# Performance work log

Measured on AMD Instinct MI355X. Metric: run time of the kernel, lower is better.

## Reference

```python
import math
import jax, jax.numpy as jnp
import numpy as np

N_HEAD = 16

def setup_inputs() -> dict:
    key = jax.random.key(0)
    k1, k2, k3 = jax.random.split(key, 3)
    B, T, C = 4, 2048, 1024
    x = jax.random.normal(k1, (B, T, C), dtype=jnp.float32)
    Wqkv = jax.random.normal(k2, (C, 3 * C), dtype=jnp.float32) * (1.0 / math.sqrt(C))
    bqkv = jnp.zeros((3 * C,), dtype=jnp.float32)
    Wproj = jax.random.normal(k3, (C, C), dtype=jnp.float32) * (1.0 / math.sqrt(C))
    bproj = jnp.zeros((C,), dtype=jnp.float32)
    return {"x": x, "Wqkv": Wqkv, "bqkv": bqkv, "Wproj": Wproj, "bproj": bproj}

def reference(x, Wqkv, bqkv, Wproj, bproj):
    B, T, C = x.shape
    H = N_HEAD
    D = C // H
    # fused QKV projection
    qkv = x @ Wqkv + bqkv                      # [B,T,3C]
    qkv = qkv.reshape(B, T, 3, H, D).transpose(0, 2, 3, 1, 4)  # [B,3,H,T,D]
    q, k, v = qkv[:, 0], qkv[:, 1], qkv[:, 2]  # each [B,H,T,D]
    scale = 1.0 / math.sqrt(D)
    att = jnp.einsum('bhtd,bhsd->bhts', q, k) * scale  # [B,H,T,T]
    # causal mask: disallow s > t
    mask = jnp.triu(jnp.ones((T, T), dtype=bool), k=1)
    att = jnp.where(mask, jnp.float32(-1e9), att)
    att = jax.nn.softmax(att, axis=-1)
    y = jnp.einsum('bhts,bhsd->bhtd', att, v)  # [B,H,T,D]
    y = y.transpose(0, 2, 1, 3).reshape(B, T, C)
    y = y @ Wproj + bproj
    return y
```

## Files before the change

kernel.cpp:

```cpp
#include <hip/hip_runtime.h>
#include <hip/hip_bf16.h>

#define B_ 4
#define T_ 2048
#define C_ 1024
#define H_ 16
#define D_ 64

typedef __attribute__((ext_vector_type(8))) short short8;
typedef __attribute__((ext_vector_type(4))) float f32x4;

#define QSCALE 0.18033688011112042f

static __device__ __forceinline__ unsigned short f2bf(float f) {
  unsigned u = __float_as_uint(f);
  u += 0x7fff + ((u >> 16) & 1);
  return (unsigned short)(u >> 16);
}

static __device__ __forceinline__ unsigned cvt_pk_bf16(float lo, float hi) {
  unsigned r;
  asm("v_cvt_pk_bf16_f32 %0, %1, %2" : "=v"(r) : "v"(lo), "v"(hi));
  return r;
}

static __device__ __forceinline__ float fast_exp2(float x) {
#if __has_builtin(__builtin_amdgcn_exp2f)
  return __builtin_amdgcn_exp2f(x);
#else
  return exp2f(x);
#endif
}

#define GL2LDS16(g, l)                                              \
  __builtin_amdgcn_global_load_lds(                                 \
      (const __attribute__((address_space(1))) void*)(g),           \
      (__attribute__((address_space(3))) void*)(l), 16, 0, 0)

__global__ __launch_bounds__(256) void prepass(
    const float* __restrict__ x, const float* __restrict__ Wq,
    const float* __restrict__ Wp, ushort* __restrict__ xb,
    ushort* __restrict__ Wqt, ushort* __restrict__ Wpt) {
  __shared__ ushort tile[32][33];
  const int bid = blockIdx.x;
  if (bid < 8192) {
    const size_t i = ((size_t)bid * 256 + threadIdx.x) * 4;
    float4 vv = *(const float4*)(x + i);
    ushort4 o = {f2bf(vv.x), f2bf(vv.y), f2bf(vv.z), f2bf(vv.w)};
    *(ushort4*)(xb + i) = o;
    return;
  }
  const float* in;
  ushort* out;
  int N, tix;
  if (bid < 8192 + 3072) {
    in = Wq; out = Wqt; N = 3 * C_; tix = bid - 8192;
  } else {
    in = Wp; out = Wpt; N = C_; tix = bid - 11264;
  }
  const int nT = N >> 5;
  const int k0 = (tix / nT) << 5, n0 = (tix % nT) << 5;
  const int r = threadIdx.x >> 3;
  const int c4 = (threadIdx.x & 7) << 2;
  float4 v = *(const float4*)(in + (size_t)(k0 + r) * N + n0 + c4);
  tile[c4 + 0][r] = f2bf(v.x);
  tile[c4 + 1][r] = f2bf(v.y);
  tile[c4 + 2][r] = f2bf(v.z);
  tile[c4 + 3][r] = f2bf(v.w);
  __syncthreads();
  ushort4 o = {tile[r][c4], tile[r][c4 + 1], tile[r][c4 + 2], tile[r][c4 + 3]};
  *(ushort4*)(out + (size_t)(n0 + r) * C_ + k0 + c4) = o;
}

static __device__ __forceinline__ void swz_src64(int wave, int lane, int p,
                                                 int& row, int& offU) {
  const int flat = p * 4096 + wave * 1024 + lane * 16;
  row = flat >> 7;
  const int pos = (flat & 127) >> 4;
  const int x = pos ^ (row & 7);
  offU = x * 8;
}
static __device__ __forceinline__ int swz_frag64(int r, int quad, int ko) {
  return r * 128 + (((quad | (ko << 2)) ^ (r & 7)) << 4);
}

__global__ __launch_bounds__(512, 2) void gemm_qkv_mfma(
    const ushort* __restrict__ A, const ushort* __restrict__ Bt,
    const float* __restrict__ bias, ushort* __restrict__ q,
    ushort* __restrict__ k, ushort* __restrict__ v) {
  __shared__ __align__(16) ushort KA[3][128 * 64];
  __shared__ __align__(16) ushort KB[3][256 * 64];
  const int wave = threadIdx.x >> 6, lane = threadIdx.x & 63;
  const int c = lane & 15, quad = lane >> 4;
  const int wm = wave >> 2, wn = wave & 3;
  const int bid0 = blockIdx.x;
  const int bid = (bid0 & 7) * 96 + (bid0 >> 3);
  const int m0 = (bid / 12) << 7;
  const int n0 = (bid % 12) << 8;

  int aRow[2], aX[2], bRow[4], bX[4];
#pragma unroll
  for (int p = 0; p < 2; ++p) {
    const int flat = p * 8192 + (int)threadIdx.x * 16;
    aRow[p] = flat >> 7;
    aX[p] = (((flat & 127) >> 4) ^ (aRow[p] & 7)) * 8;
  }
#pragma unroll
  for (int p = 0; p < 4; ++p) {
    const int flat = p * 8192 + (int)threadIdx.x * 16;
    bRow[p] = flat >> 7;
    bX[p] = (((flat & 127) >> 4) ^ (bRow[p] & 7)) * 8;
  }
  int fOffA[2][4], fOffB[2][4];
#pragma unroll
  for (int ko = 0; ko < 2; ++ko) {
#pragma unroll
    for (int i = 0; i < 4; ++i)
      fOffA[ko][i] = swz_frag64(wm * 64 + i * 16 + c, quad, ko);
#pragma unroll
    for (int j = 0; j < 4; ++j)
      fOffB[ko][j] = swz_frag64(wn * 64 + j * 16 + c, quad, ko);
  }

  f32x4 acc[4][4];
#pragma unroll
  for (int i = 0; i < 4; ++i)
#pragma unroll
    for (int j = 0; j < 4; ++j) acc[i][j] = (f32x4){0.f, 0.f, 0.f, 0.f};

#pragma unroll
  for (int p = 0; p < 4; ++p)
    GL2LDS16(Bt + (size_t)(n0 + bRow[p]) * C_ + bX[p],
             (char*)KB[0] + p * 8192 + wave * 1024);
#pragma unroll
  for (int p = 0; p < 2; ++p)
    GL2LDS16(A + (size_t)(m0 + aRow[p]) * C_ + aX[p],
             (char*)KA[0] + p * 8192 + wave * 1024);
#pragma unroll
  for (int p = 0; p < 4; ++p)
    GL2LDS16(Bt + (size_t)(n0 + bRow[p]) * C_ + 64 + bX[p],
             (char*)KB[1] + p * 8192 + wave * 1024);
#pragma unroll
  for (int p = 0; p < 2; ++p)
    GL2LDS16(A + (size_t)(m0 + aRow[p]) * C_ + 64 + aX[p],
             (char*)KA[1] + p * 8192 + wave * 1024);
  asm volatile("s_waitcnt vmcnt(6)" ::: "memory");
  __builtin_amdgcn_s_barrier();

  int cur = 0, s2 = 2;
  for (int kt = 0; kt < 16; ++kt) {
    const int kk2 = (kt + 2) << 6;
    const bool more = (kt + 2) < 16;
    const char* la = (const char*)KA[cur];
    const char* lb = (const char*)KB[cur];
    short8 af[4][2], bf0[2][2], bf1[2][2];

#pragma unroll
    for (int i = 0; i < 4; ++i)
#pragma unroll
      for (int ko = 0; ko < 2; ++ko) af[i][ko] = *(const short8*)(la + fOffA[ko][i]);
#pragma unroll
    for (int d = 0; d < 2; ++d)
#pragma unroll
      for (int ko = 0; ko < 2; ++ko) bf0[d][ko] = *(const short8*)(lb + fOffB[ko][d]);
    if (more) {
      GL2LDS16(Bt + (size_t)(n0 + bRow[0]) * C_ + kk2 + bX[0],
               (char*)KB[s2] + 0 * 8192 + wave * 1024);
      GL2LDS16(Bt + (size_t)(n0 + bRow[1]) * C_ + kk2 + bX[1],
               (char*)KB[s2] + 1 * 8192 + wave * 1024);
      GL2LDS16(A + (size_t)(m0 + aRow[0]) * C_ + kk2 + aX[0],
               (char*)KA[s2] + 0 * 8192 + wave * 1024);
    }
    __builtin_amdgcn_s_barrier();
    __builtin_amdgcn_s_setprio(1);
#pragma unroll
    for (int i = 0; i < 4; ++i)
#pragma unroll
      for (int dj = 0; dj < 2; ++dj)
#pragma unroll
        for (int ko = 0; ko < 2; ++ko)
          acc[i][dj] = __builtin_amdgcn_mfma_f32_16x16x32_bf16(
              af[i][ko], bf0[dj][ko], acc[i][dj], 0, 0, 0);
    __builtin_amdgcn_s_setprio(0);
    __builtin_amdgcn_s_barrier();

#pragma unroll
    for (int d = 0; d < 2; ++d)
#pragma unroll
      for (int ko = 0; ko < 2; ++ko)
        bf1[d][ko] = *(const short8*)(lb + fOffB[ko][2 + d]);
    if (more) {
      GL2LDS16(Bt + (size_t)(n0 + bRow[2]) * C_ + kk2 + bX[2],
               (char*)KB[s2] + 2 * 8192 + wave * 1024);
      GL2LDS16(Bt + (size_t)(n0 + bRow[3]) * C_ + kk2 + bX[3],
               (char*)KB[s2] + 3 * 8192 + wave * 1024);
      GL2LDS16(A + (size_t)(m0 + aRow[1]) * C_ + kk2 + aX[1],
               (char*)KA[s2] + 1 * 8192 + wave * 1024);
    }
    __builtin_amdgcn_s_barrier();
    __builtin_amdgcn_s_setprio(1);
#pragma unroll
    for (int i = 0; i < 4; ++i)
#pragma unroll
      for (int dj = 0; dj < 2; ++dj)
#pragma unroll
        for (int ko = 0; ko < 2; ++ko)
          acc[i][2 + dj] = __builtin_amdgcn_mfma_f32_16x16x32_bf16(
              af[i][ko], bf1[dj][ko], acc[i][2 + dj], 0, 0, 0);
    __builtin_amdgcn_s_setprio(0);
    __builtin_amdgcn_s_barrier();

    if (kt + 1 < 16) {
      if (more)
        asm volatile("s_waitcnt vmcnt(6)" ::: "memory");
      else
        asm volatile("s_waitcnt vmcnt(0)" ::: "memory");
      __builtin_amdgcn_s_barrier();
    }
    cur = (cur == 2) ? 0 : cur + 1;
    s2 = (s2 == 2) ? 0 : s2 + 1;
  }

  const int s = n0 >> 10;
  if (s == 2) {
#pragma unroll
    for (int j = 0; j < 4; ++j) {
      const int n = n0 + wn * 64 + j * 16 + c;
      const int h = (n >> 6) & 15, d = n & 63;
      const float bval = bias[n];
#pragma unroll
      for (int i = 0; i < 4; ++i) {
        const int m = m0 + wm * 64 + i * 16 + quad * 4;
        const int b = m >> 11, t = m & 2047;
        ushort4 pk = {f2bf(acc[i][j][0] + bval), f2bf(acc[i][j][1] + bval),
                      f2bf(acc[i][j][2] + bval), f2bf(acc[i][j][3] + bval)};
        *(ushort4*)(v + (((size_t)((b << 4) + h) << 6) + d) * T_ + t) = pk;
      }
    }
  } else {
    ushort* outp = (s == 0) ? q : k;
    const float sc = (s == 0) ? QSCALE : 1.0f;
#pragma unroll
    for (int j = 0; j < 4; ++j) {
      const int n = n0 + wn * 64 + j * 16 + c;
      const int h = (n >> 6) & 15, d = n & 63;
      const float bval = bias[n];
#pragma unroll
      for (int i = 0; i < 4; ++i) {
#pragma unroll
        for (int r = 0; r < 4; ++r) {
          const int m = m0 + wm * 64 + i * 16 + quad * 4 + r;
          const int b = m >> 11, t = m & 2047;
          outp[(((size_t)((b << 4) + h) << 11) + t) * 64 + d] =
              f2bf((acc[i][j][r] + bval) * sc);
        }
      }
    }
  }
}

__global__ __launch_bounds__(256) void gemm_proj_mfma(
    const ushort* __restrict__ A, const ushort* __restrict__ Bt,
    const float* __restrict__ bias, float* __restrict__ out) {
  __shared__ __align__(16) ushort As[128 * 64];
  __shared__ __align__(16) ushort Bs[128 * 64];
  const int tid = threadIdx.x;
  const int wave = tid >> 6, lane = tid & 63;
  const int c = lane & 15, quad = lane >> 4;
  const int wm = wave & 1, wn = wave >> 1;
  const int bid0 = blockIdx.y * 8 + blockIdx.x;
  const int bid = (bid0 & 7) * 64 + (bid0 >> 3);
  const int m0 = (bid >> 3) << 7;
  const int n0 = (bid & 7) << 7;

  int sRow[4], sOff[4];
#pragma unroll
  for (int p = 0; p < 4; ++p) swz_src64(wave, lane, p, sRow[p], sOff[p]);
  int fOffA[2][4], fOffB[2][4];
#pragma unroll
  for (int ko = 0; ko < 2; ++ko) {
#pragma unroll
    for (int i = 0; i < 4; ++i)
      fOffA[ko][i] = swz_frag64(wm * 64 + i * 16 + c, quad, ko);
#pragma unroll
    for (int j = 0; j < 4; ++j)
      fOffB[ko][j] = swz_frag64(wn * 64 + j * 16 + c, quad, ko);
  }

  f32x4 acc[4][4];
#pragma unroll
  for (int i = 0; i < 4; ++i)
#pragma unroll
    for (int j = 0; j < 4; ++j) acc[i][j] = (f32x4){0.f, 0.f, 0.f, 0.f};

  for (int k0 = 0; k0 < C_; k0 += 64) {
    __syncthreads();
#pragma unroll
    for (int p = 0; p < 4; ++p) {
      GL2LDS16(A + (size_t)(m0 + sRow[p]) * C_ + k0 + sOff[p],
               (char*)As + p * 4096 + wave * 1024);
      GL2LDS16(Bt + (size_t)(n0 + sRow[p]) * C_ + k0 + sOff[p],
               (char*)Bs + p * 4096 + wave * 1024);
    }
    __syncthreads();
#pragma unroll
    for (int ko = 0; ko < 2; ++ko) {
      short8 af[4], bf[4];
#pragma unroll
      for (int i = 0; i < 4; ++i)
        af[i] = *(const short8*)((const char*)As + fOffA[ko][i]);
#pragma unroll
      for (int j = 0; j < 4; ++j)
        bf[j] = *(const short8*)((const char*)Bs + fOffB[ko][j]);
#pragma unroll
      for (int i = 0; i < 4; ++i)
#pragma unroll
        for (int j = 0; j < 4; ++j)
          acc[i][j] = __builtin_amdgcn_mfma_f32_16x16x32_bf16(af[i], bf[j],
                                                              acc[i][j], 0, 0, 0);
    }
  }

#pragma unroll
  for (int j = 0; j < 4; ++j) {
    const int n = n0 + wn * 64 + j * 16 + c;
    const float bval = bias[n];
#pragma unroll
    for (int i = 0; i < 4; ++i) {
#pragma unroll
      for (int r = 0; r < 4; ++r) {
        const int m = m0 + wm * 64 + i * 16 + quad * 4 + r;
        out[(size_t)m * C_ + n] = acc[i][j][r] + bval;
      }
    }
  }
}

__global__ __launch_bounds__(256) void attn(const ushort* __restrict__ q,
                                            const ushort* __restrict__ k,
                                            const ushort* __restrict__ v,
                                            ushort* __restrict__ y2) {
  const int qt = 15 - (int)(blockIdx.x >> 6);
  const int bh = blockIdx.x & 63;
  const int t0 = qt << 7;
  const int w = threadIdx.x >> 6;
  const int lane = threadIdx.x & 63;
  const int c = lane & 15;
  const int quad = lane >> 4;

  const ushort* qp = q + (size_t)bh * T_ * D_;
  const ushort* kp = k + (size_t)bh * T_ * D_;
  const ushort* vp = v + (size_t)bh * D_ * T_;

  __shared__ __align__(16) ushort Ks[2][64 * 64];
  __shared__ __align__(16) ushort Vs[2][64 * 64];
  __shared__ __align__(16) ushort Ps[4][32][72];

  short8 qf[2][2];
#pragma unroll
  for (int g = 0; g < 2; ++g) {
    const ushort* qrow = qp + (size_t)(t0 + 32 * w + 16 * g + c) * D_;
    qf[g][0] = *(const short8*)(qrow + quad * 8);
    qf[g][1] = *(const short8*)(qrow + 32 + quad * 8);
  }

  int sRow[2], sX[2];
#pragma unroll
  for (int p = 0; p < 2; ++p) {
    const int flat = p * 4096 + (int)threadIdx.x * 16;
    sRow[p] = flat >> 7;
    sX[p] = (((flat & 127) >> 4) ^ (sRow[p] & 7)) * 8;
  }

#define STAGE(buf, s0s)                                                   \
  do {                                                                    \
    _Pragma("unroll") for (int p = 0; p < 2; ++p) {                       \
      GL2LDS16(kp + (size_t)((s0s) + sRow[p]) * D_ + sX[p],               \
               (char*)Ks[buf] + p * 4096 + w * 1024);                     \
      GL2LDS16(vp + (size_t)sRow[p] * T_ + (s0s) + sX[p],                 \
               (char*)Vs[buf] + p * 4096 + w * 1024);                     \
    }                                                                     \
  } while (0)

  f32x4 o[2][4];
  float l_i[2] = {0.f, 0.f};
#pragma unroll
  for (int g = 0; g < 2; ++g)
#pragma unroll
    for (int dt = 0; dt < 4; ++dt) o[g][dt] = (f32x4){0.f, 0.f, 0.f, 0.f};

  const int nb = 2 * qt + 2;
  STAGE(0, 0);
  int cur = 0;

  for (int ib = 0; ib < nb; ++ib) {
    const int s0 = ib << 6;
    __syncthreads();
    if (ib + 1 < nb) STAGE(cur ^ 1, s0 + 64);

    f32x4 st[2][4];
    __builtin_amdgcn_s_setprio(1);
#pragma unroll
    for (int kt = 0; kt < 4; ++kt) {
      const char* kb = (const char*)Ks[cur];
      short8 af0 = *(const short8*)(kb + swz_frag64(kt * 16 + c, quad, 0));
      short8 af1 = *(const short8*)(kb + swz_frag64(kt * 16 + c, quad, 1));
#pragma unroll
      for (int g = 0; g < 2; ++g) {
        f32x4 a = (f32x4){0.f, 0.f, 0.f, 0.f};
        a = __builtin_amdgcn_mfma_f32_16x16x32_bf16(af0, qf[g][0], a, 0, 0, 0);
        a = __builtin_amdgcn_mfma_f32_16x16x32_bf16(af1, qf[g][1], a, 0, 0, 0);
        st[g][kt] = a;
      }
    }
    __builtin_amdgcn_s_setprio(0);

#pragma unroll
    for (int g = 0; g < 2; ++g) {
      const int qbase = t0 + 32 * w + 16 * g;
      if (s0 + 63 > qbase) {
#pragma unroll
        for (int kt = 0; kt < 4; ++kt)
#pragma unroll
          for (int r = 0; r < 4; ++r)
            if (s0 + kt * 16 + 4 * quad + r > qbase + c) st[g][kt][r] = -1e30f;
      }
      float lacc = 0.f;
#pragma unroll
      for (int kt = 0; kt < 4; ++kt) {
        float p0 = fast_exp2(st[g][kt][0]);
        float p1 = fast_exp2(st[g][kt][1]);
        float p2 = fast_exp2(st[g][kt][2]);
        float p3 = fast_exp2(st[g][kt][3]);
        lacc += (p0 + p1) + (p2 + p3);
        uint2 pw = {cvt_pk_bf16(p0, p1), cvt_pk_bf16(p2, p3)};
        *(uint2*)(&Ps[w][g * 16 + c][kt * 16 + 4 * quad]) = pw;
      }
      l_i[g] += lacc;
    }

    short8 pf[2][2];
#pragma unroll
    for (int g = 0; g < 2; ++g) {
      pf[g][0] = *(const short8*)(&Ps[w][g * 16 + c][quad * 8]);
      pf[g][1] = *(const short8*)(&Ps[w][g * 16 + c][32 + quad * 8]);
    }
    __builtin_amdgcn_s_setprio(1);
#pragma unroll
    for (int dt = 0; dt < 4; ++dt) {
      const char* vb = (const char*)Vs[cur];
      short8 vf0 = *(const short8*)(vb + swz_frag64(dt * 16 + c, quad, 0));
      short8 vf1 = *(const short8*)(vb + swz_frag64(dt * 16 + c, quad, 1));
#pragma unroll
      for (int g = 0; g < 2; ++g) {
        o[g][dt] =
            __builtin_amdgcn_mfma_f32_16x16x32_bf16(vf0, pf[g][0], o[g][dt], 0, 0, 0);
        o[g][dt] =
            __builtin_amdgcn_mfma_f32_16x16x32_bf16(vf1, pf[g][1], o[g][dt], 0, 0, 0);
      }
    }
    __builtin_amdgcn_s_setprio(0);
    cur ^= 1;
  }
#undef STAGE

  float linv[2];
#pragma unroll
  for (int g = 0; g < 2; ++g) {
    float ls = l_i[g];
    ls += __shfl_xor(ls, 16);
    ls += __shfl_xor(ls, 32);
    linv[g] = 1.0f / ls;
  }

  const int b = bh >> 4, h = bh & 15;
#pragma unroll
  for (int g = 0; g < 2; ++g) {
    const int row = t0 + 32 * w + 16 * g + c;
    ushort* dst = y2 + (size_t)(b * T_ + row) * C_ + h * 64;
#pragma unroll
    for (int dt = 0; dt < 4; ++dt) {
      uint2 ov = {cvt_pk_bf16(o[g][dt][0] * linv[g], o[g][dt][1] * linv[g]),
                  cvt_pk_bf16(o[g][dt][2] * linv[g], o[g][dt][3] * linv[g])};
      *(uint2*)(dst + dt * 16 + 4 * quad) = ov;
    }
  }
}

extern "C" void kernel_launch(void* const* d_in, const int* in_sizes, int n_in,
                              void* d_out, int out_size, void* d_ws,
                              size_t ws_size, hipStream_t stream) {
  const float* x = (const float*)d_in[0];
  const float* Wqkv = (const float*)d_in[1];
  const float* bqkv = (const float*)d_in[2];
  const float* Wproj = (const float*)d_in[3];
  const float* bproj = (const float*)d_in[4];
  float* out = (float*)d_out;

  const size_t per = (size_t)B_ * H_ * T_ * D_;
  ushort* q = (ushort*)d_ws;
  ushort* k = q + per;
  ushort* v = k + per;
  ushort* y2 = v + per;
  ushort* xb = y2 + per;
  ushort* Wqkvt = xb + per;
  ushort* Wprojt = Wqkvt + 3 * C_ * C_;

  prepass<<<dim3(12288), 256, 0, stream>>>(x, Wqkv, Wproj, xb, Wqkvt, Wprojt);
  gemm_qkv_mfma<<<dim3(768), 512, 0, stream>>>(xb, Wqkvt, bqkv, q, k, v);
  attn<<<dim3(1024), 256, 0, stream>>>(q, k, v, y2);
  gemm_proj_mfma<<<dim3(8, 64), 256, 0, stream>>>(y2, Wprojt, bproj, out);
}
```

Measured before the change: 258.8 us.

## Double-buffer proj GEMM loads and shuffle P fragments instead of LDS roundtrip

The output-projection GEMM now double-buffers its A/B tiles in shared memory, so the next k-tile is prefetched while MFMAs run on the current one. It also raises wave priority around the MFMA block, and one barrier per iteration is removed. In the attention kernel, the softmax probability tile no longer goes through a per-wave LDS scratch buffer; the MFMA input fragments are rebuilt with cross-lane shuffles instead. The changes double the GEMM's LDS footprint, which may reduce occupancy, and add shuffle and select instructions in the attention inner loop.

```diff
diff --git a/kernel.cpp b/kernel.cpp
--- a/kernel.cpp
+++ b/kernel.cpp
@@ -262,8 +262,8 @@
 __global__ __launch_bounds__(256) void gemm_proj_mfma(
     const ushort* __restrict__ A, const ushort* __restrict__ Bt,
     const float* __restrict__ bias, float* __restrict__ out) {
-  __shared__ __align__(16) ushort As[128 * 64];
-  __shared__ __align__(16) ushort Bs[128 * 64];
+  __shared__ __align__(16) ushort As[2][128 * 64];
+  __shared__ __align__(16) ushort Bs[2][128 * 64];
   const int tid = threadIdx.x;
   const int wave = tid >> 6, lane = tid & 63;
   const int c = lane & 15, quad = lane >> 4;
@@ -293,33 +293,42 @@
 #pragma unroll
     for (int j = 0; j < 4; ++j) acc[i][j] = (f32x4){0.f, 0.f, 0.f, 0.f};
 
+#define PROJ_STAGE(buf, kk)                                            \
+  do {                                                                 \
+    _Pragma("unroll") for (int p = 0; p < 4; ++p) {                    \
+      GL2LDS16(A + (size_t)(m0 + sRow[p]) * C_ + (kk) + sOff[p],       \
+               (char*)As[buf] + p * 4096 + wave * 1024);               \
+      GL2LDS16(Bt + (size_t)(n0 + sRow[p]) * C_ + (kk) + sOff[p],      \
+               (char*)Bs[buf] + p * 4096 + wave * 1024);               \
+    }                                                                  \
+  } while (0)
+
+  PROJ_STAGE(0, 0);
+  int cur = 0;
   for (int k0 = 0; k0 < C_; k0 += 64) {
     __syncthreads();
-#pragma unroll
-    for (int p = 0; p < 4; ++p) {
-      GL2LDS16(A + (size_t)(m0 + sRow[p]) * C_ + k0 + sOff[p],
-               (char*)As + p * 4096 + wave * 1024);
-      GL2LDS16(Bt + (size_t)(n0 + sRow[p]) * C_ + k0 + sOff[p],
-               (char*)Bs + p * 4096 + wave * 1024);
-    }
-    __syncthreads();
+    if (k0 + 64 < C_) PROJ_STAGE(cur ^ 1, k0 + 64);
 #pragma unroll
     for (int ko = 0; ko < 2; ++ko) {
       short8 af[4], bf[4];
 #pragma unroll
       for (int i = 0; i < 4; ++i)
-        af[i] = *(const short8*)((const char*)As + fOffA[ko][i]);
+        af[i] = *(const short8*)((const char*)As[cur] + fOffA[ko][i]);
 #pragma unroll
       for (int j = 0; j < 4; ++j)
-        bf[j] = *(const short8*)((const char*)Bs + fOffB[ko][j]);
+        bf[j] = *(const short8*)((const char*)Bs[cur] + fOffB[ko][j]);
+      __builtin_amdgcn_s_setprio(1);
 #pragma unroll
       for (int i = 0; i < 4; ++i)
 #pragma unroll
         for (int j = 0; j < 4; ++j)
           acc[i][j] = __builtin_amdgcn_mfma_f32_16x16x32_bf16(af[i], bf[j],
                                                               acc[i][j], 0, 0, 0);
-    }
-  }
+      __builtin_amdgcn_s_setprio(0);
+    }
+    cur ^= 1;
+  }
+#undef PROJ_STAGE
 
 #pragma unroll
   for (int j = 0; j < 4; ++j) {
@@ -354,7 +363,6 @@
 
   __shared__ __align__(16) ushort Ks[2][64 * 64];
   __shared__ __align__(16) ushort Vs[2][64 * 64];
-  __shared__ __align__(16) ushort Ps[4][32][72];
 
   short8 qf[2][2];
 #pragma unroll
@@ -392,6 +400,8 @@
   const int nb = 2 * qt + 2;
   STAGE(0, 0);
   int cur = 0;
+  const int sA = c + ((quad & 1) << 5);
+  const int sB = sA + 16;
 
   for (int ib = 0; ib < nb; ++ib) {
     const int s0 = ib << 6;
@@ -415,6 +425,7 @@
     }
     __builtin_amdgcn_s_setprio(0);
 
+    unsigned pw[2][4][2];
 #pragma unroll
     for (int g = 0; g < 2; ++g) {
       const int qbase = t0 + 32 * w + 16 * g;
@@ -433,8 +444,8 @@
         float p2 = fast_exp2(st[g][kt][2]);
         float p3 = fast_exp2(st[g][kt][3]);
         lacc += (p0 + p1) + (p2 + p3);
-        uint2 pw = {cvt_pk_bf16(p0, p1), cvt_pk_bf16(p2, p3)};
-        *(uint2*)(&Ps[w][g * 16 + c][kt * 16 + 4 * quad]) = pw;
+        pw[g][kt][0] = cvt_pk_bf16(p0, p1);
+        pw[g][kt][1] = cvt_pk_bf16(p2, p3);
       }
       l_i[g] += lacc;
     }
@@ -442,9 +453,27 @@
     short8 pf[2][2];
 #pragma unroll
     for (int g = 0; g < 2; ++g) {
-      pf[g][0] = *(const short8*)(&Ps[w][g * 16 + c][quad * 8]);
-      pf[g][1] = *(const short8*)(&Ps[w][g * 16 + c][32 + quad * 8]);
-    }
+#pragma unroll
+      for (int half = 0; half < 2; ++half) {
+        const unsigned lo0 = pw[g][half * 2][0], lo1 = pw[g][half * 2][1];
+        const unsigned hi0 = pw[g][half * 2 + 1][0], hi1 = pw[g][half * 2 + 1][1];
+        const unsigned a0 = (unsigned)__shfl((int)lo0, sA);
+        const unsigned b0 = (unsigned)__shfl((int)hi0, sA);
+        const unsigned a1 = (unsigned)__shfl((int)lo1, sA);
+        const unsigned b1 = (unsigned)__shfl((int)hi1, sA);
+        const unsigned a2 = (unsigned)__shfl((int)lo0, sB);
+        const unsigned b2 = (unsigned)__shfl((int)hi0, sB);
+        const unsigned a3 = (unsigned)__shfl((int)lo1, sB);
+        const unsigned b3 = (unsigned)__shfl((int)hi1, sB);
+        uint4 r;
+        r.x = (quad & 2) ? b0 : a0;
+        r.y = (quad & 2) ? b1 : a1;
+        r.z = (quad & 2) ? b2 : a2;
+        r.w = (quad & 2) ? b3 : a3;
+        pf[g][half] = *(short8*)&r;
+      }
+    }
+
     __builtin_amdgcn_s_setprio(1);
 #pragma unroll
     for (int dt = 0; dt < 4; ++dt) {
```

Result: faster. 249.3 us (-3.7%).
